# Optimization experiments

Hardware: AMD Instinct MI355X
Metric: run time of the kernel (lower is better)

Reference implementation:

```python
import jax, jax.numpy as jnp
import numpy as np

B, T, DIM = 2, 2048, 2048
N_HEADS, N_KV_HEADS = 32, 8
HEAD_DIM = DIM // N_HEADS          # 64
N_REP = N_HEADS // N_KV_HEADS      # 4
ROPE_THETA = 10000.0


def setup_inputs() -> dict:
    key = jax.random.key(0)
    ks = jax.random.split(key, 5)
    x = jax.random.normal(ks[0], (B, T, DIM), dtype=jnp.float32)
    # RoPE frequencies: freqs_cis[t, j] = exp(i * t * theta^{-2j/head_dim})
    inv_freq = 1.0 / (ROPE_THETA ** (jnp.arange(0, HEAD_DIM, 2, dtype=jnp.float32) / HEAD_DIM))
    angles = jnp.arange(T, dtype=jnp.float32)[:, None] * inv_freq[None, :]  # [T, HEAD_DIM//2]
    cos, sin = jnp.cos(angles), jnp.sin(angles)
    s = 0.02
    wq = jax.random.normal(ks[1], (N_HEADS * HEAD_DIM, DIM), dtype=jnp.float32) * s
    wk = jax.random.normal(ks[2], (N_KV_HEADS * HEAD_DIM, DIM), dtype=jnp.float32) * s
    wv = jax.random.normal(ks[3], (N_KV_HEADS * HEAD_DIM, DIM), dtype=jnp.float32) * s
    wo = jax.random.normal(ks[4], (DIM, DIM), dtype=jnp.float32) * s
    return {"x": x, "cos": cos, "sin": sin, "wq": wq, "wk": wk, "wv": wv, "wo": wo}


def _apply_rope(t, cos, sin):
    # t: [B, T, H, D]; cos/sin: [T, D//2]. Complex multiply on interleaved pairs.
    b, tt, h, d = t.shape
    tr = t.reshape(b, tt, h, d // 2, 2)
    t0, t1 = tr[..., 0], tr[..., 1]
    c = cos[None, :, None, :]
    s = sin[None, :, None, :]
    o0 = t0 * c - t1 * s
    o1 = t0 * s + t1 * c
    return jnp.stack([o0, o1], axis=-1).reshape(b, tt, h, d)


def reference(x, cos, sin, wq, wk, wv, wo):
    Bs, Ts, C = x.shape
    # Projections (nn.Linear, no bias): y = x @ W^T
    q = jnp.einsum('btc,oc->bto', x, wq).reshape(Bs, Ts, N_HEADS, HEAD_DIM)
    k = jnp.einsum('btc,oc->bto', x, wk).reshape(Bs, Ts, N_KV_HEADS, HEAD_DIM)
    v = jnp.einsum('btc,oc->bto', x, wv).reshape(Bs, Ts, N_KV_HEADS, HEAD_DIM)
    q = _apply_rope(q, cos[:Ts], sin[:Ts])
    k = _apply_rope(k, cos[:Ts], sin[:Ts])
    # [B, H, T, D]; GQA: broadcast kv heads via grouped einsum instead of repeat.
    q = q.transpose(0, 2, 1, 3).reshape(Bs, N_KV_HEADS, N_REP, Ts, HEAD_DIM)
    k = k.transpose(0, 2, 1, 3)  # [B, Hkv, T, D]
    v = v.transpose(0, 2, 1, 3)
    scale = 1.0 / jnp.sqrt(jnp.asarray(HEAD_DIM, dtype=x.dtype))
    scores = jnp.einsum('bgrqd,bgkd->bgrqk', q, k) * scale  # [B, Hkv, rep, T, T]
    causal = jnp.tril(jnp.ones((Ts, Ts), dtype=bool))
    scores = jnp.where(causal, scores, jnp.finfo(scores.dtype).min)
    attn = jax.nn.softmax(scores, axis=-1)
    y = jnp.einsum('bgrqk,bgkd->bgrqd', attn, v)           # [B, Hkv, rep, T, D]
    y = y.reshape(Bs, N_HEADS, Ts, HEAD_DIM).transpose(0, 2, 1, 3).reshape(Bs, Ts, C)
    return jnp.einsum('btc,oc->bto', y, wo)
```

## Files before the change

### kernel.cpp

```cpp
#include <hip/hip_runtime.h>

typedef __bf16 bf16;
typedef __attribute__((ext_vector_type(8))) __bf16 bf16x8;
typedef __attribute__((ext_vector_type(4))) __bf16 bf16x4;
typedef __attribute__((ext_vector_type(4))) float f32x4;

constexpr int T_SEQ = 2048;
constexpr int DIM   = 2048;
constexpr int NH    = 32;
constexpr int NKV   = 8;
constexpr int HD    = 64;
constexpr int QKV_N = DIM + 2 * NKV * HD;
constexpr int MROWS = 2 * T_SEQ;

__global__ void cast_kernel(const float* __restrict__ in, bf16* __restrict__ out, int n) {
  int stride = gridDim.x * blockDim.x * 4;
  for (int i = (blockIdx.x * blockDim.x + threadIdx.x) * 4; i < n; i += stride) {
    float4 v = *(const float4*)(in + i);
    bf16x4 o = { (bf16)v.x, (bf16)v.y, (bf16)v.z, (bf16)v.w };
    *(bf16x4*)(out + i) = o;
  }
}

__global__ void cast_w_kernel(const float* __restrict__ wq, const float* __restrict__ wk,
                              const float* __restrict__ wv, const float* __restrict__ wo,
                              bf16* __restrict__ wqkv, bf16* __restrict__ wob) {
  int stride = gridDim.x * blockDim.x;
  for (int g = blockIdx.x * blockDim.x + threadIdx.x; g < 2621440; g += stride) {
    const float* src; bf16* dst; int off;
    if (g < 1048576)      { src = wq; dst = wqkv;           off = g; }
    else if (g < 1310720) { src = wk; dst = wqkv + 4194304; off = g - 1048576; }
    else if (g < 1572864) { src = wv; dst = wqkv + 5242880; off = g - 1310720; }
    else                  { src = wo; dst = wob;            off = g - 1572864; }
    float4 v = *(const float4*)(src + (size_t)off * 4);
    bf16x4 o = { (bf16)v.x, (bf16)v.y, (bf16)v.z, (bf16)v.w };
    *(bf16x4*)(dst + (size_t)off * 4) = o;
  }
}

template <typename OutT>
__global__ __launch_bounds__(512) void gemm256(const bf16* __restrict__ A,
                                               const bf16* __restrict__ W,
                                               OutT* __restrict__ C,
                                               int N, int K, int cpx) {
  constexpr int BM = 256, BN = 128, BK = 64;
  __shared__ __attribute__((aligned(16))) bf16 Ab[3][BM * BK];
  __shared__ __attribute__((aligned(16))) bf16 Bb[3][BN * BK];
  const int tid = threadIdx.x, lane = tid & 63, wave = tid >> 6;
  const int l15 = lane & 15, l4 = lane >> 4;
  const int orig = blockIdx.x;
  const int wg = (orig & 7) * cpx + (orig >> 3);
  const int bm = (wg & 15) * BM;
  const int bn = (wg >> 4) * BN;
  const int wm = (wave >> 1) * 64, wn = (wave & 1) * 64;

  f32x4 acc[4][4] = {};

  const int NT = K / BK;
  auto stage = [&](int s, int k0) {
    #pragma unroll
    for (int i = 0; i < 4; ++i) {
      int c = i * 512 + tid;
      int row = c >> 3;
      int gc = ((c & 7) ^ (row & 7)) << 3;
      __builtin_amdgcn_global_load_lds(
          (const __attribute__((address_space(1))) unsigned int*)(A + (size_t)(bm + row) * K + k0 + gc),
          (__attribute__((address_space(3))) unsigned int*)(&Ab[s][0] + c * 8), 16, 0, 0);
    }
    #pragma unroll
    for (int i = 0; i < 2; ++i) {
      int c = i * 512 + tid;
      int row = c >> 3;
      int gc = ((c & 7) ^ (row & 7)) << 3;
      __builtin_amdgcn_global_load_lds(
          (const __attribute__((address_space(1))) unsigned int*)(W + (size_t)(bn + row) * K + k0 + gc),
          (__attribute__((address_space(3))) unsigned int*)(&Bb[s][0] + c * 8), 16, 0, 0);
    }
  };

  stage(0, 0);
  stage(1, BK);

  int d = 0;
  for (int t = 0; t < NT; ++t) {
    if (t + 1 < NT) { asm volatile("s_waitcnt vmcnt(6)" ::: "memory"); }
    else            { asm volatile("s_waitcnt vmcnt(0)" ::: "memory"); }
    __builtin_amdgcn_s_barrier();

    bf16x8 af[2][4], bfr[2][4];
    #pragma unroll
    for (int kk = 0; kk < 2; ++kk) {
      #pragma unroll
      for (int mi = 0; mi < 4; ++mi) {
        int row = wm + mi * 16 + l15;
        af[kk][mi] = *(const bf16x8*)((const char*)&Ab[d][0] + row * 128 +
                                      (((kk * 4 + l4) ^ (row & 7)) << 4));
      }
      #pragma unroll
      for (int ni = 0; ni < 4; ++ni) {
        int row = wn + ni * 16 + l15;
        bfr[kk][ni] = *(const bf16x8*)((const char*)&Bb[d][0] + row * 128 +
                                       (((kk * 4 + l4) ^ (row & 7)) << 4));
      }
    }

    if (t + 2 < NT) {
      int s = d + 2; if (s >= 3) s -= 3;
      stage(s, (t + 2) * BK);
    }

    __builtin_amdgcn_s_setprio(1);
    #pragma unroll
    for (int kk = 0; kk < 2; ++kk)
      #pragma unroll
      for (int mi = 0; mi < 4; ++mi)
        #pragma unroll
        for (int ni = 0; ni < 4; ++ni)
          acc[mi][ni] = __builtin_amdgcn_mfma_f32_16x16x32_bf16(af[kk][mi], bfr[kk][ni],
                                                                acc[mi][ni], 0, 0, 0);
    __builtin_amdgcn_s_setprio(0);

    ++d; if (d == 3) d = 0;
  }

  #pragma unroll
  for (int mi = 0; mi < 4; ++mi)
    #pragma unroll
    for (int ni = 0; ni < 4; ++ni) {
      size_t row = (size_t)bm + wm + mi * 16 + l4 * 4;
      int col = bn + wn + ni * 16 + l15;
      #pragma unroll
      for (int r = 0; r < 4; ++r)
        C[(row + r) * N + col] = (OutT)acc[mi][ni][r];
    }
}

__global__ void rope_kernel(bf16* __restrict__ qkv, const float* __restrict__ cs,
                            const float* __restrict__ sn) {
  int idx = blockIdx.x * blockDim.x + threadIdx.x;
  int m = idx / 160;
  int ch = idx - m * 160;
  int t = m & (T_SEQ - 1);
  int col, c;
  if (ch < 128) { int hh = ch >> 2; c = ch & 3; col = hh * 64 + c * 16; }
  else          { int ch2 = ch - 128; int hh = ch2 >> 2; c = ch2 & 3; col = DIM + hh * 64 + c * 16; }
  bf16* ptr = qkv + (size_t)m * QKV_N + col;
  bf16x8 v0 = *(bf16x8*)ptr, v1 = *(bf16x8*)(ptr + 8);
  const float* cp = cs + t * 32 + c * 8;
  const float* sp = sn + t * 32 + c * 8;
  float4 c0 = *(const float4*)cp, c1 = *(const float4*)(cp + 4);
  float4 s0 = *(const float4*)sp, s1 = *(const float4*)(sp + 4);
  float cc[8] = {c0.x, c0.y, c0.z, c0.w, c1.x, c1.y, c1.z, c1.w};
  float ss[8] = {s0.x, s0.y, s0.z, s0.w, s1.x, s1.y, s1.z, s1.w};
  bf16x8 o0, o1;
  #pragma unroll
  for (int j = 0; j < 4; ++j) {
    float a = (float)v0[2 * j], b = (float)v0[2 * j + 1];
    o0[2 * j]     = (bf16)(a * cc[j] - b * ss[j]);
    o0[2 * j + 1] = (bf16)(a * ss[j] + b * cc[j]);
  }
  #pragma unroll
  for (int j = 0; j < 4; ++j) {
    float a = (float)v1[2 * j], b = (float)v1[2 * j + 1];
    o1[2 * j]     = (bf16)(a * cc[4 + j] - b * ss[4 + j]);
    o1[2 * j + 1] = (bf16)(a * ss[4 + j] + b * cc[4 + j]);
  }
  *(bf16x8*)ptr = o0;
  *(bf16x8*)(ptr + 8) = o1;
}

__global__ __launch_bounds__(512, 4) void attn_kernel(const bf16* __restrict__ qkv,
                                                      bf16* __restrict__ y) {
  const int h = blockIdx.x, b = blockIdx.z;
  const int strip = 15 - blockIdx.y;
  const int g = h >> 2;
  const int tid = threadIdx.x, lane = tid & 63, wave = tid >> 6;
  const int l15 = lane & 15, l4 = lane >> 4;
  const int qbase = strip * 128 + wave * 16;

  __shared__ __attribute__((aligned(16))) bf16 Kb[2][64 * 64];
  __shared__ __attribute__((aligned(16))) bf16 VTs[2][64 * 64];
  __shared__ __attribute__((aligned(16))) bf16 Pb[8][16 * 64];

  constexpr float SCALE2 = 0.125f * 1.44269504088896f;
  constexpr float THR_RAW = 8.0f / SCALE2;

  bf16x8 qf[2];
  {
    const bf16* qp = qkv + ((size_t)b * T_SEQ + qbase + l15) * QKV_N + h * HD + l4 * 8;
    qf[0] = *(const bf16x8*)(qp);
    qf[1] = *(const bf16x8*)(qp + 32);
  }

  f32x4 oacc[4] = {};
  float m_run = -INFINITY, l_run = 0.f;

  const int last_kt = (qbase + 15) >> 6;
  const int nt_loop = 2 * strip + 2;
  const size_t kvbase = (size_t)b * T_SEQ;

  {
    int r = tid >> 3;
    int csrc = ((tid & 7) << 3) ^ ((r & 7) << 3);
    __builtin_amdgcn_global_load_lds(
        (const __attribute__((address_space(1))) unsigned int*)
            (qkv + (kvbase + r) * QKV_N + DIM + g * HD + csrc),
        (__attribute__((address_space(3))) unsigned int*)(&Kb[0][0] + tid * 8), 16, 0, 0);
    const bf16* vp = qkv + (kvbase + wave * 8) * QKV_N + DIM + NKV * HD + g * HD + lane;
    bf16x8 vr;
    #pragma unroll
    for (int j = 0; j < 8; ++j) vr[j] = vp[(size_t)j * QKV_N];
    *(bf16x8*)((char*)&VTs[0][0] + ((lane * 128 + wave * 16) ^ ((lane & 7) << 4))) = vr;
    asm volatile("s_waitcnt vmcnt(0)" ::: "memory");
    __syncthreads();
  }

  int cur = 0;
  for (int kt = 0; kt < nt_loop; ++kt) {
    const bool has_next = (kt + 1) < nt_loop;
    bf16x8 vr;
    if (has_next) {
      int r = tid >> 3;
      int csrc = ((tid & 7) << 3) ^ ((r & 7) << 3);
      __builtin_amdgcn_global_load_lds(
          (const __attribute__((address_space(1))) unsigned int*)
              (qkv + (kvbase + (kt + 1) * 64 + r) * QKV_N + DIM + g * HD + csrc),
          (__attribute__((address_space(3))) unsigned int*)(&Kb[cur ^ 1][0] + tid * 8), 16, 0, 0);
      const bf16* vp = qkv + (kvbase + (kt + 1) * 64 + wave * 8) * QKV_N
                           + DIM + NKV * HD + g * HD + lane;
      #pragma unroll
      for (int j = 0; j < 8; ++j) vr[j] = vp[(size_t)j * QKV_N];
    }

    if (kt <= last_kt) {
      const bf16* kb = &Kb[cur][0];
      const bf16* vt = &VTs[cur][0];

      f32x4 z[4];
      #pragma unroll
      for (int nt = 0; nt < 4; ++nt) z[nt] = (f32x4){0.f, 0.f, 0.f, 0.f};
      #pragma unroll
      for (int nt = 0; nt < 4; ++nt)
        #pragma unroll
        for (int kk = 0; kk < 2; ++kk) {
          bf16x8 kf = *(const bf16x8*)((const char*)kb +
              (((nt * 16 + l15) * 128 + (kk * 32 + l4 * 8) * 2) ^ ((l15 & 7) << 4)));
          z[nt] = __builtin_amdgcn_mfma_f32_16x16x32_bf16(kf, qf[kk], z[nt], 0, 0, 0);
        }

      if (kt == last_kt) {
        const int qg = qbase + l15;
        #pragma unroll
        for (int nt = 0; nt < 4; ++nt)
          #pragma unroll
          for (int r = 0; r < 4; ++r)
            if (kt * 64 + nt * 16 + l4 * 4 + r > qg) z[nt][r] = -INFINITY;
      }

      float vm = z[0][0];
      #pragma unroll
      for (int nt = 0; nt < 4; ++nt)
        #pragma unroll
        for (int r = 0; r < 4; ++r) vm = fmaxf(vm, z[nt][r]);
      vm = fmaxf(vm, __shfl_xor(vm, 16));
      vm = fmaxf(vm, __shfl_xor(vm, 32));

      if (!__all(vm - m_run <= THR_RAW)) {
        float mnew = fmaxf(m_run, vm);
        float alpha = __builtin_amdgcn_exp2f((m_run - mnew) * SCALE2);
        l_run *= alpha;
        #pragma unroll
        for (int dt = 0; dt < 4; ++dt)
          #pragma unroll
          for (int r = 0; r < 4; ++r) oacc[dt][r] *= alpha;
        m_run = mnew;
      }
      const float ms = m_run * SCALE2;

      float ps = 0.f;
      #pragma unroll
      for (int nt = 0; nt < 4; ++nt)
        #pragma unroll
        for (int r = 0; r < 4; ++r) {
          float pv = __builtin_amdgcn_exp2f(__builtin_fmaf(z[nt][r], SCALE2, -ms));
          z[nt][r] = pv;
          ps += pv;
        }
      ps += __shfl_xor(ps, 16);
      ps += __shfl_xor(ps, 32);
      l_run += ps;

      bf16* pbw = &Pb[wave][0];
      #pragma unroll
      for (int nt = 0; nt < 4; ++nt) {
        bf16x4 pk = { (bf16)z[nt][0], (bf16)z[nt][1], (bf16)z[nt][2], (bf16)z[nt][3] };
        *(bf16x4*)((char*)pbw + ((l15 * 128 + nt * 32 + l4 * 8) ^ ((l15 & 7) << 4))) = pk;
      }

      #pragma unroll
      for (int kk = 0; kk < 2; ++kk) {
        bf16x8 pf = *(const bf16x8*)((const char*)pbw +
            ((l15 * 128 + kk * 64 + l4 * 16) ^ ((l15 & 7) << 4)));
        #pragma unroll
        for (int dt = 0; dt < 4; ++dt) {
          bf16x8 vf = *(const bf16x8*)((const char*)vt +
              (((dt * 16 + l15) * 128 + (kk * 32 + l4 * 8) * 2) ^ ((l15 & 7) << 4)));
          oacc[dt] = __builtin_amdgcn_mfma_f32_16x16x32_bf16(vf, pf, oacc[dt], 0, 0, 0);
        }
      }
    }

    if (has_next) {
      *(bf16x8*)((char*)&VTs[cur ^ 1][0] + ((lane * 128 + wave * 16) ^ ((lane & 7) << 4))) = vr;
      asm volatile("s_waitcnt vmcnt(0)" ::: "memory");
      __syncthreads();
      cur ^= 1;
    }
  }

  {
    float linv = __builtin_amdgcn_rcpf(l_run);
    bf16* yp = y + ((size_t)b * T_SEQ + qbase + l15) * DIM + h * HD + l4 * 4;
    #pragma unroll
    for (int dt = 0; dt < 4; ++dt) {
      bf16x4 ov = { (bf16)(oacc[dt][0] * linv), (bf16)(oacc[dt][1] * linv),
                    (bf16)(oacc[dt][2] * linv), (bf16)(oacc[dt][3] * linv) };
      *(bf16x4*)(yp + dt * 16) = ov;
    }
  }
}

extern "C" void kernel_launch(void* const* d_in, const int* in_sizes, int n_in,
                              void* d_out, int out_size, void* d_ws, size_t ws_size,
                              hipStream_t stream) {
  const float* x    = (const float*)d_in[0];
  const float* cosb = (const float*)d_in[1];
  const float* sinb = (const float*)d_in[2];
  const float* wq   = (const float*)d_in[3];
  const float* wk   = (const float*)d_in[4];
  const float* wv   = (const float*)d_in[5];
  const float* wo   = (const float*)d_in[6];
  float* out = (float*)d_out;

  bf16* xb   = (bf16*)d_ws;
  bf16* wqkv = xb + (size_t)MROWS * DIM;
  bf16* wob  = wqkv + (size_t)QKV_N * DIM;
  bf16* qkv  = wob + (size_t)DIM * DIM;
  bf16* y    = qkv + (size_t)MROWS * QKV_N;

  cast_kernel<<<2048, 256, 0, stream>>>(x, xb, MROWS * DIM);
  cast_w_kernel<<<2048, 256, 0, stream>>>(wq, wk, wv, wo, wqkv, wob);

  gemm256<bf16><<<384, 512, 0, stream>>>(xb, wqkv, qkv, QKV_N, DIM, 384 / 8);

  rope_kernel<<<(MROWS * 160) / 256, 256, 0, stream>>>(qkv, cosb, sinb);

  attn_kernel<<<dim3(NH, 16, 2), 512, 0, stream>>>(qkv, y);

  gemm256<float><<<256, 512, 0, stream>>>(y, wob, out, DIM, DIM, 256 / 8);
}
```

Measured before the change: 192.8 us.

## Process 128-row KV tiles per attention loop iteration with single-buffered V

The attention kernel now stages 128 K rows per iteration (double-buffered) and splits them into two 64-row halves. V for both halves is kept in a single buffer, which needs an extra barrier before it is overwritten. This halves the number of loop iterations and barrier rounds. On the diagonal tile, waves whose queries cannot see the upper half skip that half, and the per-tile last_kt check is gone. Launch bounds drop from 4 to 2 blocks per CU, allowing more registers at the cost of occupancy. The extra barrier and the larger LDS footprint (about 64KB per block) are the trade-offs.

New measurement: 185.6 us. 3.7% less time.

```diff
diff --git a/kernel.cpp b/kernel.cpp
--- a/kernel.cpp
+++ b/kernel.cpp
@@ -169,7 +169,7 @@
   *(bf16x8*)(ptr + 8) = o1;
 }
 
-__global__ __launch_bounds__(512, 4) void attn_kernel(const bf16* __restrict__ qkv,
+__global__ __launch_bounds__(512, 2) void attn_kernel(const bf16* __restrict__ qkv,
                                                       bf16* __restrict__ y) {
   const int h = blockIdx.x, b = blockIdx.z;
   const int strip = 15 - blockIdx.y;
@@ -178,12 +178,13 @@
   const int l15 = lane & 15, l4 = lane >> 4;
   const int qbase = strip * 128 + wave * 16;
 
-  __shared__ __attribute__((aligned(16))) bf16 Kb[2][64 * 64];
+  __shared__ __attribute__((aligned(16))) bf16 Kb[2][128 * 64];
   __shared__ __attribute__((aligned(16))) bf16 VTs[2][64 * 64];
   __shared__ __attribute__((aligned(16))) bf16 Pb[8][16 * 64];
 
   constexpr float SCALE2 = 0.125f * 1.44269504088896f;
   constexpr float THR_RAW = 8.0f / SCALE2;
+  constexpr int VOFF = DIM + NKV * HD;
 
   bf16x8 qf[2];
   {
@@ -194,74 +195,89 @@
 
   f32x4 oacc[4] = {};
   float m_run = -INFINITY, l_run = 0.f;
-
-  const int last_kt = (qbase + 15) >> 6;
-  const int nt_loop = 2 * strip + 2;
+  const int qg = qbase + l15;
+
+  const int nt = strip + 1;
   const size_t kvbase = (size_t)b * T_SEQ;
 
   {
-    int r = tid >> 3;
-    int csrc = ((tid & 7) << 3) ^ ((r & 7) << 3);
-    __builtin_amdgcn_global_load_lds(
-        (const __attribute__((address_space(1))) unsigned int*)
-            (qkv + (kvbase + r) * QKV_N + DIM + g * HD + csrc),
-        (__attribute__((address_space(3))) unsigned int*)(&Kb[0][0] + tid * 8), 16, 0, 0);
-    const bf16* vp = qkv + (kvbase + wave * 8) * QKV_N + DIM + NKV * HD + g * HD + lane;
-    bf16x8 vr;
-    #pragma unroll
-    for (int j = 0; j < 8; ++j) vr[j] = vp[(size_t)j * QKV_N];
-    *(bf16x8*)((char*)&VTs[0][0] + ((lane * 128 + wave * 16) ^ ((lane & 7) << 4))) = vr;
+    #pragma unroll
+    for (int i = 0; i < 2; ++i) {
+      int chunk = i * 512 + tid;
+      int row = chunk >> 3;
+      int csrc = ((chunk & 7) << 3) ^ ((row & 7) << 3);
+      __builtin_amdgcn_global_load_lds(
+          (const __attribute__((address_space(1))) unsigned int*)
+              (qkv + (kvbase + row) * QKV_N + DIM + g * HD + csrc),
+          (__attribute__((address_space(3))) unsigned int*)(&Kb[0][0] + chunk * 8), 16, 0, 0);
+    }
+    #pragma unroll
+    for (int hf = 0; hf < 2; ++hf) {
+      const bf16* vp = qkv + (kvbase + hf * 64 + wave * 8) * QKV_N + VOFF + g * HD + lane;
+      bf16x8 vr;
+      #pragma unroll
+      for (int j = 0; j < 8; ++j) vr[j] = vp[(size_t)j * QKV_N];
+      *(bf16x8*)((char*)&VTs[hf][0] + ((lane * 128 + wave * 16) ^ ((lane & 7) << 4))) = vr;
+    }
     asm volatile("s_waitcnt vmcnt(0)" ::: "memory");
     __syncthreads();
   }
 
   int cur = 0;
-  for (int kt = 0; kt < nt_loop; ++kt) {
-    const bool has_next = (kt + 1) < nt_loop;
-    bf16x8 vr;
+  for (int kt = 0; kt < nt; ++kt) {
+    const bool has_next = (kt + 1) < nt;
+    bf16x8 vr0, vr1;
     if (has_next) {
-      int r = tid >> 3;
-      int csrc = ((tid & 7) << 3) ^ ((r & 7) << 3);
-      __builtin_amdgcn_global_load_lds(
-          (const __attribute__((address_space(1))) unsigned int*)
-              (qkv + (kvbase + (kt + 1) * 64 + r) * QKV_N + DIM + g * HD + csrc),
-          (__attribute__((address_space(3))) unsigned int*)(&Kb[cur ^ 1][0] + tid * 8), 16, 0, 0);
-      const bf16* vp = qkv + (kvbase + (kt + 1) * 64 + wave * 8) * QKV_N
-                           + DIM + NKV * HD + g * HD + lane;
-      #pragma unroll
-      for (int j = 0; j < 8; ++j) vr[j] = vp[(size_t)j * QKV_N];
-    }
-
-    if (kt <= last_kt) {
-      const bf16* kb = &Kb[cur][0];
-      const bf16* vt = &VTs[cur][0];
+      #pragma unroll
+      for (int i = 0; i < 2; ++i) {
+        int chunk = i * 512 + tid;
+        int row = chunk >> 3;
+        int csrc = ((chunk & 7) << 3) ^ ((row & 7) << 3);
+        __builtin_amdgcn_global_load_lds(
+            (const __attribute__((address_space(1))) unsigned int*)
+                (qkv + (kvbase + (kt + 1) * 128 + row) * QKV_N + DIM + g * HD + csrc),
+            (__attribute__((address_space(3))) unsigned int*)(&Kb[cur ^ 1][0] + chunk * 8), 16, 0, 0);
+      }
+      const bf16* vp0 = qkv + (kvbase + (kt + 1) * 128 + wave * 8) * QKV_N + VOFF + g * HD + lane;
+      const bf16* vp1 = vp0 + (size_t)64 * QKV_N;
+      #pragma unroll
+      for (int j = 0; j < 8; ++j) vr0[j] = vp0[(size_t)j * QKV_N];
+      #pragma unroll
+      for (int j = 0; j < 8; ++j) vr1[j] = vp1[(size_t)j * QKV_N];
+    }
+
+    const bf16* kb = &Kb[cur][0];
+    const bool diag = (kt == strip);
+
+    #pragma unroll
+    for (int hf = 0; hf < 2; ++hf) {
+      if (diag && hf == 1 && wave < 4) continue;
 
       f32x4 z[4];
       #pragma unroll
-      for (int nt = 0; nt < 4; ++nt) z[nt] = (f32x4){0.f, 0.f, 0.f, 0.f};
-      #pragma unroll
-      for (int nt = 0; nt < 4; ++nt)
+      for (int nt4 = 0; nt4 < 4; ++nt4) z[nt4] = (f32x4){0.f, 0.f, 0.f, 0.f};
+      #pragma unroll
+      for (int nt4 = 0; nt4 < 4; ++nt4)
         #pragma unroll
         for (int kk = 0; kk < 2; ++kk) {
           bf16x8 kf = *(const bf16x8*)((const char*)kb +
-              (((nt * 16 + l15) * 128 + (kk * 32 + l4 * 8) * 2) ^ ((l15 & 7) << 4)));
-          z[nt] = __builtin_amdgcn_mfma_f32_16x16x32_bf16(kf, qf[kk], z[nt], 0, 0, 0);
+              (((hf * 64 + nt4 * 16 + l15) * 128 + (kk * 32 + l4 * 8) * 2) ^ ((l15 & 7) << 4)));
+          z[nt4] = __builtin_amdgcn_mfma_f32_16x16x32_bf16(kf, qf[kk], z[nt4], 0, 0, 0);
         }
 
-      if (kt == last_kt) {
-        const int qg = qbase + l15;
-        #pragma unroll
-        for (int nt = 0; nt < 4; ++nt)
+      if (diag) {
+        #pragma unroll
+        for (int nt4 = 0; nt4 < 4; ++nt4)
           #pragma unroll
           for (int r = 0; r < 4; ++r)
-            if (kt * 64 + nt * 16 + l4 * 4 + r > qg) z[nt][r] = -INFINITY;
+            if (kt * 128 + hf * 64 + nt4 * 16 + l4 * 4 + r > qg) z[nt4][r] = -INFINITY;
       }
 
       float vm = z[0][0];
       #pragma unroll
-      for (int nt = 0; nt < 4; ++nt)
-        #pragma unroll
-        for (int r = 0; r < 4; ++r) vm = fmaxf(vm, z[nt][r]);
+      for (int nt4 = 0; nt4 < 4; ++nt4)
+        #pragma unroll
+        for (int r = 0; r < 4; ++r) vm = fmaxf(vm, z[nt4][r]);
       vm = fmaxf(vm, __shfl_xor(vm, 16));
       vm = fmaxf(vm, __shfl_xor(vm, 32));
 
@@ -279,11 +295,11 @@
 
       float ps = 0.f;
       #pragma unroll
-      for (int nt = 0; nt < 4; ++nt)
+      for (int nt4 = 0; nt4 < 4; ++nt4)
         #pragma unroll
         for (int r = 0; r < 4; ++r) {
-          float pv = __builtin_amdgcn_exp2f(__builtin_fmaf(z[nt][r], SCALE2, -ms));
-          z[nt][r] = pv;
+          float pv = __builtin_amdgcn_exp2f(__builtin_fmaf(z[nt4][r], SCALE2, -ms));
+          z[nt4][r] = pv;
           ps += pv;
         }
       ps += __shfl_xor(ps, 16);
@@ -292,11 +308,12 @@
 
       bf16* pbw = &Pb[wave][0];
       #pragma unroll
-      for (int nt = 0; nt < 4; ++nt) {
-        bf16x4 pk = { (bf16)z[nt][0], (bf16)z[nt][1], (bf16)z[nt][2], (bf16)z[nt][3] };
-        *(bf16x4*)((char*)pbw + ((l15 * 128 + nt * 32 + l4 * 8) ^ ((l15 & 7) << 4))) = pk;
-      }
-
+      for (int nt4 = 0; nt4 < 4; ++nt4) {
+        bf16x4 pk = { (bf16)z[nt4][0], (bf16)z[nt4][1], (bf16)z[nt4][2], (bf16)z[nt4][3] };
+        *(bf16x4*)((char*)pbw + ((l15 * 128 + nt4 * 32 + l4 * 8) ^ ((l15 & 7) << 4))) = pk;
+      }
+
+      const bf16* vt = &VTs[hf][0];
       #pragma unroll
       for (int kk = 0; kk < 2; ++kk) {
         bf16x8 pf = *(const bf16x8*)((const char*)pbw +
@@ -311,8 +328,9 @@
     }
 
     if (has_next) {
-      *(bf16x8*)((char*)&VTs[cur ^ 1][0] + ((lane * 128 + wave * 16) ^ ((lane & 7) << 4))) = vr;
-      asm volatile("s_waitcnt vmcnt(0)" ::: "memory");
+      __syncthreads();
+      *(bf16x8*)((char*)&VTs[0][0] + ((lane * 128 + wave * 16) ^ ((lane & 7) << 4))) = vr0;
+      *(bf16x8*)((char*)&VTs[1][0] + ((lane * 128 + wave * 16) ^ ((lane & 7) << 4))) = vr1;
       __syncthreads();
       cur ^= 1;
     }
```
